# Performance work log

Measured on AMD Instinct MI355X. Metric: run time of the kernel, lower is better.

The kernel has to match this reference:

```python
import jax, jax.numpy as jnp
import numpy as np

ALPHA = 0.2          # LeakyReLU negative slope
NEG_INF = -9e15      # mask fill value from the original module


def setup_inputs() -> dict:
    key = jax.random.key(0)
    k1, k2, k3, k4, k5, k6 = jax.random.split(key, 6)
    N, E, F_in, F_out = 1024, 32768, 128, 128
    h = jax.random.normal(k1, (N, F_in), dtype=jnp.float32)
    edge_attr = jax.random.normal(k2, (E, F_in), dtype=jnp.float32)
    adjacency = jax.random.randint(k3, (N, N), 0, 2, dtype=jnp.int32)
    node2node_features = jax.random.normal(k4, (N * N, F_in), dtype=jnp.float32)
    # learned params (xavier_uniform with gain=1.414)
    def xavier(k, shape, gain=1.414):
        fan_in, fan_out = shape[0], shape[1]
        bound = gain * np.sqrt(6.0 / (fan_in + fan_out))
        return jax.random.uniform(k, shape, jnp.float32, -bound, bound)
    W = xavier(k5, (F_in, F_out))
    a = xavier(k6, (3 * F_out, 1))
    return {"h": h, "edge_attr": edge_attr, "adjacency": adjacency,
            "node2node_features": node2node_features, "W": W, "a": a}


def reference(h, edge_attr, adjacency, node2node_features, W, a):
    N = h.shape[0]
    F_out = W.shape[1]
    Wh = h @ W  # [N, F_out]
    # a_input[i,j] = concat(Wh[i], Wh[j], (n2n@W)[i*N+j]); matmul with a decomposes:
    a1, a2, a3 = a[:F_out, 0], a[F_out:2 * F_out, 0], a[2 * F_out:, 0]
    s1 = Wh @ a1                                   # [N]
    s2 = Wh @ a2                                   # [N]
    s3 = (node2node_features @ (W @ a3)).reshape(N, N)
    e = jax.nn.leaky_relu(s1[:, None] + s2[None, :] + s3, negative_slope=ALPHA)
    masked = jnp.where(adjacency > 0, e, NEG_INF)
    attention = jax.nn.softmax(masked, axis=1)
    h_prime = jax.nn.elu(attention @ Wh)           # concat=True branch
    edge_out = jax.nn.elu(edge_attr @ W)
    return (h_prime, edge_out)
```

## Files before the change

kernel.cpp:

```cpp
#include <hip/hip_runtime.h>
#include <hip/hip_bf16.h>

#define ALPHA 0.2f
#define NEG_INF -9000000000000000.0f

#define N_NODES 1024
#define F_DIM   128
#define E_EDGES 32768
#define NN      (N_NODES * N_NODES)

typedef float f32x4 __attribute__((ext_vector_type(4)));

__global__ __launch_bounds__(256) void k_wh(const float* __restrict__ h,
                                            const float* __restrict__ W,
                                            float* __restrict__ Wh) {
    int idx = blockIdx.x * 256 + threadIdx.x;
    int i = idx >> 7;
    int f = idx & 127;
    const float* hrow = h + i * 128;
    float acc = 0.f;
#pragma unroll 16
    for (int k = 0; k < 128; ++k)
        acc = fmaf(hrow[k], W[k * 128 + f], acc);
    Wh[idx] = acc;
}

__global__ __launch_bounds__(64) void k_vecs(const float* __restrict__ Wh,
                                             const float* __restrict__ W,
                                             const float* __restrict__ a,
                                             float* __restrict__ s1,
                                             float* __restrict__ s2,
                                             float* __restrict__ v3) {
    int b = blockIdx.x;
    int lane = threadIdx.x;
    if (b < N_NODES) {
        const float* row = Wh + b * 128;
        float x0 = row[lane], x1 = row[lane + 64];
        float p1 = fmaf(x0, a[lane],       x1 * a[lane + 64]);
        float p2 = fmaf(x0, a[128 + lane], x1 * a[192 + lane]);
#pragma unroll
        for (int off = 32; off; off >>= 1) {
            p1 += __shfl_xor(p1, off);
            p2 += __shfl_xor(p2, off);
        }
        if (lane == 0) { s1[b] = p1; s2[b] = p2; }
    } else {
        int i = b - N_NODES;
        const float* row = W + i * 128;
        float p = fmaf(row[lane], a[256 + lane], row[lane + 64] * a[320 + lane]);
#pragma unroll
        for (int off = 32; off; off >>= 1) p += __shfl_xor(p, off);
        if (lane == 0) v3[i] = p;
    }
}

__global__ __launch_bounds__(256) void k_s3(const float* __restrict__ n2n,
                                            const float* __restrict__ v3,
                                            const float* __restrict__ s1,
                                            const float* __restrict__ s2,
                                            const int* __restrict__ adj,
                                            float* __restrict__ emask) {
    int tid  = threadIdx.x;
    int lane = tid & 63;
    int wave = tid >> 6;
    int sub  = lane & 31;
    int half = lane >> 5;

    f32x4 v = ((const f32x4*)v3)[sub];

    long long base = (long long)blockIdx.x * 32;

    int keep[4];
#pragma unroll
    for (int c = 0; c < 4; ++c)
        keep[c] = adj[base + c * 8 + wave * 2 + half];

#pragma unroll
    for (int c = 0; c < 4; ++c) {
        long long r = base + c * 8 + wave * 2 + half;
        float val = 0.f;
        if (keep[c] > 0) {
            const f32x4* rowp = (const f32x4*)(n2n + r * 128);
            f32x4 x = __builtin_nontemporal_load(rowp + sub);
            val = fmaf(x.x, v.x, fmaf(x.y, v.y, fmaf(x.z, v.z, x.w * v.w)));
        }
        val += __shfl_xor(val, 16);
        val += __shfl_xor(val, 8);
        val += __shfl_xor(val, 4);
        val += __shfl_xor(val, 2);
        val += __shfl_xor(val, 1);
        if (sub == 0) {
            float o = NEG_INF;
            if (keep[c] > 0) {
                int i = (int)(r >> 10);
                int j = (int)(r & 1023);
                float e = s1[i] + s2[j] + val;
                o = e > 0.f ? e : ALPHA * e;
            }
            __builtin_nontemporal_store(o, emask + r);
        }
    }
}

#define ROWS_PER_BLK 4
__global__ __launch_bounds__(256) void k_attn(const float* __restrict__ emask,
                                              const float* __restrict__ Wh,
                                              float* __restrict__ out) {
    __shared__ float att[ROWS_PER_BLK][1024];
    __shared__ float red[4];
    __shared__ float4 part[8][32];
    __shared__ float rsum[ROWS_PER_BLK];

    int tid = threadIdx.x;
    int i0 = blockIdx.x * ROWS_PER_BLK;

    for (int r = 0; r < ROWS_PER_BLK; ++r) {
        const float* erow = emask + (long long)(i0 + r) * 1024;
        float v0 = erow[tid];
        float v1 = erow[tid + 256];
        float v2 = erow[tid + 512];
        float v3r = erow[tid + 768];
        float m = fmaxf(fmaxf(v0, v1), fmaxf(v2, v3r));
#pragma unroll
        for (int off = 32; off; off >>= 1) m = fmaxf(m, __shfl_xor(m, off));
        if ((tid & 63) == 0) red[tid >> 6] = m;
        __syncthreads();
        m = fmaxf(fmaxf(red[0], red[1]), fmaxf(red[2], red[3]));
        __syncthreads();

        float e0 = expf(v0 - m), e1 = expf(v1 - m), e2 = expf(v2 - m), e3 = expf(v3r - m);
        att[r][tid] = e0; att[r][tid + 256] = e1; att[r][tid + 512] = e2; att[r][tid + 768] = e3;
        float s = e0 + e1 + e2 + e3;
#pragma unroll
        for (int off = 32; off; off >>= 1) s += __shfl_xor(s, off);
        if ((tid & 63) == 0) red[tid >> 6] = s;
        __syncthreads();
        if (tid == 0) rsum[r] = 1.0f / (red[0] + red[1] + red[2] + red[3]);
        __syncthreads();
    }

    int f4 = tid & 31;
    int slice = tid >> 5;
    const float4* WhV = (const float4*)Wh;
    float4 acc[ROWS_PER_BLK];
#pragma unroll
    for (int r = 0; r < ROWS_PER_BLK; ++r) acc[r] = make_float4(0.f, 0.f, 0.f, 0.f);
    int jbase = slice * 128;
    for (int jj = 0; jj < 128; ++jj) {
        int j = jbase + jj;
        float4 w = WhV[j * 32 + f4];
#pragma unroll
        for (int r = 0; r < ROWS_PER_BLK; ++r) {
            float aw = att[r][j];
            acc[r].x = fmaf(aw, w.x, acc[r].x);
            acc[r].y = fmaf(aw, w.y, acc[r].y);
            acc[r].z = fmaf(aw, w.z, acc[r].z);
            acc[r].w = fmaf(aw, w.w, acc[r].w);
        }
    }

    for (int r = 0; r < ROWS_PER_BLK; ++r) {
        part[slice][f4] = acc[r];
        __syncthreads();
        if (tid < 32) {
            float4 t = part[0][tid];
#pragma unroll
            for (int sl = 1; sl < 8; ++sl) {
                float4 p = part[sl][tid];
                t.x += p.x; t.y += p.y; t.z += p.z; t.w += p.w;
            }
            float rs = rsum[r];
            t.x *= rs; t.y *= rs; t.z *= rs; t.w *= rs;
            t.x = t.x > 0.f ? t.x : expm1f(t.x);
            t.y = t.y > 0.f ? t.y : expm1f(t.y);
            t.z = t.z > 0.f ? t.z : expm1f(t.z);
            t.w = t.w > 0.f ? t.w : expm1f(t.w);
            ((float4*)(out + (long long)(i0 + r) * 128))[tid] = t;
        }
        __syncthreads();
    }
}

__global__ __launch_bounds__(256) void k_edge(const float* __restrict__ ea,
                                              const float* __restrict__ W,
                                              float* __restrict__ out) {
    __shared__ float Wlds[128 * 128];
    __shared__ float elds[64 * 128];
    int tid = threadIdx.x;

    {
        const float4* Wv = (const float4*)W;
        float4* Wl = (float4*)Wlds;
#pragma unroll
        for (int t = tid; t < 4096; t += 256) Wl[t] = Wv[t];
        long long rowbase = (long long)blockIdx.x * 64;
        const float4* ev = (const float4*)(ea + rowbase * 128);
        float4* el = (float4*)elds;
#pragma unroll
        for (int t = tid; t < 2048; t += 256) el[t] = ev[t];
    }
    __syncthreads();

    int f4 = tid & 31;
    int rg = tid >> 5;
    float4 acc[8];
#pragma unroll
    for (int r = 0; r < 8; ++r) acc[r] = make_float4(0.f, 0.f, 0.f, 0.f);

    for (int k4 = 0; k4 < 32; ++k4) {
        float4 w0 = *(const float4*)&Wlds[(k4 * 4 + 0) * 128 + f4 * 4];
        float4 w1 = *(const float4*)&Wlds[(k4 * 4 + 1) * 128 + f4 * 4];
        float4 w2 = *(const float4*)&Wlds[(k4 * 4 + 2) * 128 + f4 * 4];
        float4 w3 = *(const float4*)&Wlds[(k4 * 4 + 3) * 128 + f4 * 4];
#pragma unroll
        for (int r = 0; r < 8; ++r) {
            float4 e4 = *(const float4*)&elds[(rg * 8 + r) * 128 + k4 * 4];
            acc[r].x = fmaf(e4.x, w0.x, fmaf(e4.y, w1.x, fmaf(e4.z, w2.x, fmaf(e4.w, w3.x, acc[r].x))));
            acc[r].y = fmaf(e4.x, w0.y, fmaf(e4.y, w1.y, fmaf(e4.z, w2.y, fmaf(e4.w, w3.y, acc[r].y))));
            acc[r].z = fmaf(e4.x, w0.z, fmaf(e4.y, w1.z, fmaf(e4.z, w2.z, fmaf(e4.w, w3.z, acc[r].z))));
            acc[r].w = fmaf(e4.x, w0.w, fmaf(e4.y, w1.w, fmaf(e4.z, w2.w, fmaf(e4.w, w3.w, acc[r].w))));
        }
    }

    long long rowbase = (long long)blockIdx.x * 64 + rg * 8;
#pragma unroll
    for (int r = 0; r < 8; ++r) {
        float4 t = acc[r];
        t.x = t.x > 0.f ? t.x : expm1f(t.x);
        t.y = t.y > 0.f ? t.y : expm1f(t.y);
        t.z = t.z > 0.f ? t.z : expm1f(t.z);
        t.w = t.w > 0.f ? t.w : expm1f(t.w);
        *(float4*)&out[(long long)N_NODES * F_DIM + (rowbase + r) * 128 + f4 * 4] = t;
    }
}

extern "C" void kernel_launch(void* const* d_in, const int* in_sizes, int n_in,
                              void* d_out, int out_size, void* d_ws, size_t ws_size,
                              hipStream_t stream) {
    const float* h   = (const float*)d_in[0];
    const float* ea  = (const float*)d_in[1];
    const int*   adj = (const int*)d_in[2];
    const float* n2n = (const float*)d_in[3];
    const float* W   = (const float*)d_in[4];
    const float* a   = (const float*)d_in[5];
    float* out = (float*)d_out;

    float* ws = (float*)d_ws;
    float* Wh    = ws;
    float* s1    = Wh + 131072;
    float* s2    = s1 + 1024;
    float* v3    = s2 + 1024;
    float* emask = v3 + 128;

    k_wh  <<<512,  256, 0, stream>>>(h, W, Wh);
    k_vecs<<<1152, 64,  0, stream>>>(Wh, W, a, s1, s2, v3);
    k_s3  <<<NN / 32, 256, 0, stream>>>(n2n, v3, s1, s2, adj, emask);
    k_attn<<<N_NODES / ROWS_PER_BLK, 256, 0, stream>>>(emask, Wh, out);
    k_edge<<<E_EDGES / 64, 256, 0, stream>>>(ea, W, out);
}
```

Measured before the change: 739.3 us.

## Fuse Wh projection with score vectors and double edge-GEMM rows per block

Merges the Wh matmul kernel and the s1/s2/v3 reduction kernel into one launch, where each 64-thread block computes one Wh row and immediately reduces it against a1/a2, and a single extra block computes v3 = W·a3. This removes one launch and the Wh re-read. The edge GEMM now processes 128 rows per block instead of 64, amortising the per-block W load into LDS over twice as many rows. In exchange it uses 128 KB of LDS and 16 float4 accumulators per thread, which lowers occupancy and raises register pressure.

New measurement: 739.9 us. No clear change (+0.1%).

```diff
diff --git a/kernel.cpp b/kernel.cpp
--- a/kernel.cpp
+++ b/kernel.cpp
@@ -11,33 +11,28 @@
 
 typedef float f32x4 __attribute__((ext_vector_type(4)));
 
-__global__ __launch_bounds__(256) void k_wh(const float* __restrict__ h,
+__global__ __launch_bounds__(64) void k_pre(const float* __restrict__ h,
                                             const float* __restrict__ W,
-                                            float* __restrict__ Wh) {
-    int idx = blockIdx.x * 256 + threadIdx.x;
-    int i = idx >> 7;
-    int f = idx & 127;
-    const float* hrow = h + i * 128;
-    float acc = 0.f;
-#pragma unroll 16
-    for (int k = 0; k < 128; ++k)
-        acc = fmaf(hrow[k], W[k * 128 + f], acc);
-    Wh[idx] = acc;
-}
-
-__global__ __launch_bounds__(64) void k_vecs(const float* __restrict__ Wh,
-                                             const float* __restrict__ W,
-                                             const float* __restrict__ a,
-                                             float* __restrict__ s1,
-                                             float* __restrict__ s2,
-                                             float* __restrict__ v3) {
+                                            const float* __restrict__ a,
+                                            float* __restrict__ Wh,
+                                            float* __restrict__ s1,
+                                            float* __restrict__ s2,
+                                            float* __restrict__ v3) {
     int b = blockIdx.x;
     int lane = threadIdx.x;
     if (b < N_NODES) {
-        const float* row = Wh + b * 128;
-        float x0 = row[lane], x1 = row[lane + 64];
-        float p1 = fmaf(x0, a[lane],       x1 * a[lane + 64]);
-        float p2 = fmaf(x0, a[128 + lane], x1 * a[192 + lane]);
+        const float* hrow = h + b * 128;
+        float acc0 = 0.f, acc1 = 0.f;
+#pragma unroll 8
+        for (int k = 0; k < 128; ++k) {
+            float hk = hrow[k];
+            acc0 = fmaf(hk, W[k * 128 + lane],      acc0);
+            acc1 = fmaf(hk, W[k * 128 + lane + 64], acc1);
+        }
+        Wh[b * 128 + lane]      = acc0;
+        Wh[b * 128 + lane + 64] = acc1;
+        float p1 = fmaf(acc0, a[lane],       acc1 * a[lane + 64]);
+        float p2 = fmaf(acc0, a[128 + lane], acc1 * a[192 + lane]);
 #pragma unroll
         for (int off = 32; off; off >>= 1) {
             p1 += __shfl_xor(p1, off);
@@ -45,12 +40,15 @@
         }
         if (lane == 0) { s1[b] = p1; s2[b] = p2; }
     } else {
-        int i = b - N_NODES;
-        const float* row = W + i * 128;
-        float p = fmaf(row[lane], a[256 + lane], row[lane + 64] * a[320 + lane]);
-#pragma unroll
-        for (int off = 32; off; off >>= 1) p += __shfl_xor(p, off);
-        if (lane == 0) v3[i] = p;
+        float q0 = 0.f, q1 = 0.f;
+#pragma unroll 8
+        for (int k = 0; k < 128; ++k) {
+            float a3k = a[256 + k];
+            q0 = fmaf(W[lane * 128 + k],        a3k, q0);
+            q1 = fmaf(W[(lane + 64) * 128 + k], a3k, q1);
+        }
+        v3[lane]      = q0;
+        v3[lane + 64] = q1;
     }
 }
 
@@ -185,7 +183,7 @@
                                               const float* __restrict__ W,
                                               float* __restrict__ out) {
     __shared__ float Wlds[128 * 128];
-    __shared__ float elds[64 * 128];
+    __shared__ float elds[128 * 128];
     int tid = threadIdx.x;
 
     {
@@ -193,19 +191,19 @@
         float4* Wl = (float4*)Wlds;
 #pragma unroll
         for (int t = tid; t < 4096; t += 256) Wl[t] = Wv[t];
-        long long rowbase = (long long)blockIdx.x * 64;
+        long long rowbase = (long long)blockIdx.x * 128;
         const float4* ev = (const float4*)(ea + rowbase * 128);
         float4* el = (float4*)elds;
 #pragma unroll
-        for (int t = tid; t < 2048; t += 256) el[t] = ev[t];
+        for (int t = tid; t < 4096; t += 256) el[t] = ev[t];
     }
     __syncthreads();
 
     int f4 = tid & 31;
     int rg = tid >> 5;
-    float4 acc[8];
-#pragma unroll
-    for (int r = 0; r < 8; ++r) acc[r] = make_float4(0.f, 0.f, 0.f, 0.f);
+    float4 acc[16];
+#pragma unroll
+    for (int r = 0; r < 16; ++r) acc[r] = make_float4(0.f, 0.f, 0.f, 0.f);
 
     for (int k4 = 0; k4 < 32; ++k4) {
         float4 w0 = *(const float4*)&Wlds[(k4 * 4 + 0) * 128 + f4 * 4];
@@ -213,8 +211,8 @@
         float4 w2 = *(const float4*)&Wlds[(k4 * 4 + 2) * 128 + f4 * 4];
         float4 w3 = *(const float4*)&Wlds[(k4 * 4 + 3) * 128 + f4 * 4];
 #pragma unroll
-        for (int r = 0; r < 8; ++r) {
-            float4 e4 = *(const float4*)&elds[(rg * 8 + r) * 128 + k4 * 4];
+        for (int r = 0; r < 16; ++r) {
+            float4 e4 = *(const float4*)&elds[(rg * 16 + r) * 128 + k4 * 4];
             acc[r].x = fmaf(e4.x, w0.x, fmaf(e4.y, w1.x, fmaf(e4.z, w2.x, fmaf(e4.w, w3.x, acc[r].x))));
             acc[r].y = fmaf(e4.x, w0.y, fmaf(e4.y, w1.y, fmaf(e4.z, w2.y, fmaf(e4.w, w3.y, acc[r].y))));
             acc[r].z = fmaf(e4.x, w0.z, fmaf(e4.y, w1.z, fmaf(e4.z, w2.z, fmaf(e4.w, w3.z, acc[r].z))));
@@ -222,9 +220,9 @@
         }
     }
 
-    long long rowbase = (long long)blockIdx.x * 64 + rg * 8;
-#pragma unroll
-    for (int r = 0; r < 8; ++r) {
+    long long rowbase = (long long)blockIdx.x * 128 + rg * 16;
+#pragma unroll
+    for (int r = 0; r < 16; ++r) {
         float4 t = acc[r];
         t.x = t.x > 0.f ? t.x : expm1f(t.x);
         t.y = t.y > 0.f ? t.y : expm1f(t.y);
@@ -252,9 +250,8 @@
     float* v3    = s2 + 1024;
     float* emask = v3 + 128;
 
-    k_wh  <<<512,  256, 0, stream>>>(h, W, Wh);
-    k_vecs<<<1152, 64,  0, stream>>>(Wh, W, a, s1, s2, v3);
+    k_pre <<<N_NODES + 1, 64, 0, stream>>>(h, W, a, Wh, s1, s2, v3);
     k_s3  <<<NN / 32, 256, 0, stream>>>(n2n, v3, s1, s2, adj, emask);
     k_attn<<<N_NODES / ROWS_PER_BLK, 256, 0, stream>>>(emask, Wh, out);
-    k_edge<<<E_EDGES / 64, 256, 0, stream>>>(ea, W, out);
-}
+    k_edge<<<E_EDGES / 128, 256, 0, stream>>>(ea, W, out);
+}
```
